# Kernel tuning notes

Hardware: AMD Instinct MI355X
Metric: run time of the kernel (lower is better)

The kernel has to match this reference:

```python
import jax, jax.numpy as jnp
import numpy as np
from jax import lax

# hyperparameters (match init_kwargs)
N_INP, N_HID, N_OUT = 3, 64, 10
SEQ_LEN, N_ROLL, K = 8, 16, 3
DT, GAMMA, EPS = 0.042, 2.7, 4.7
H, W = 12, 10            # hard-coded in coRNNCell2's PixelwiseConv2d
PAD = (K - 1) // 2
BATCH = 16


def setup_inputs() -> dict:
    key = jax.random.key(0)
    ks = jax.random.split(key, 7)
    x = jax.random.normal(ks[0], (SEQ_LEN, BATCH, N_INP, H, W), dtype=jnp.float32)
    # readin: Conv2d(seq_len*n_inp -> 2*n_hid, k, padding=1, replicate)
    readin_w = jax.random.normal(ks[1], (2 * N_HID, SEQ_LEN * N_INP, K, K), dtype=jnp.float32) * 0.05
    readin_b = jax.random.normal(ks[2], (2 * N_HID,), dtype=jnp.float32) * 0.05
    # PixelwiseConv2d: per-output-pixel weights (out, in, k, k, H, W)
    pw_w = jax.random.normal(ks[3], (N_HID, 2 * N_HID, K, K, H, W), dtype=jnp.float32) * 0.05
    pw_b = jax.random.normal(ks[4], (N_HID, H, W), dtype=jnp.float32) * 0.05
    # readout: 1x1 conv (n_hid -> n_out)
    readout_w = jax.random.normal(ks[5], (N_OUT, N_HID), dtype=jnp.float32) * 0.05
    readout_b = jax.random.normal(ks[6], (N_OUT,), dtype=jnp.float32) * 0.05
    return {"x": x, "readin_w": readin_w, "readin_b": readin_b,
            "pw_w": pw_w, "pw_b": pw_b,
            "readout_w": readout_w, "readout_b": readout_b}


def _pixelwise_conv(x, pw_w, pw_b):
    # x: (B, 2*N_HID, H, W); zero padding like F.unfold(padding=PAD)
    B = x.shape[0]
    xp = jnp.pad(x, ((0, 0), (0, 0), (PAD, PAD), (PAD, PAD)))
    # patches ordered (c, i, j) to match unfold().view(B, C, k, k, H, W)
    patches = jnp.stack([xp[:, :, i:i + H, j:j + W]
                         for i in range(K) for j in range(K)], axis=2)
    patches = patches.reshape(B, 2 * N_HID, K, K, H, W)
    return jnp.einsum('bcijhw,ocijhw->bohw', patches, pw_w) + pw_b[None]


def reference(x, readin_w, readin_b, pw_w, pw_b, readout_w, readout_b):
    T, B = x.shape[0], x.shape[1]
    # 't b c h w -> b (t c) h w'
    xr = jnp.transpose(x, (1, 0, 2, 3, 4)).reshape(B, T * N_INP, H, W)
    # readin conv with replicate padding
    xr_p = jnp.pad(xr, ((0, 0), (0, 0), (PAD, PAD), (PAD, PAD)), mode='edge')
    h = lax.conv_general_dilated(xr_p, readin_w, (1, 1), 'VALID',
                                 dimension_numbers=('NCHW', 'OIHW', 'NCHW'))
    h = h + readin_b[None, :, None, None]
    hy, hz = h[:, :N_HID], h[:, N_HID:]

    def step(carry, _):
        hy, hz = carry
        pre = _pixelwise_conv(jnp.concatenate([hz, hy], axis=1), pw_w, pw_b)
        hz = hz + DT * (jnp.tanh(pre) - GAMMA * hy - EPS * hz)
        hy = hy + DT * hz
        return (hy, hz), None

    (hy, hz), _ = lax.scan(step, (hy, hz), None, length=N_ROLL)
    out = jnp.einsum('bchw,oc->bohw', hy, readout_w) + readout_b[None, :, None, None]
    return out
```

## Files before the change

### kernel.cpp

```cpp
#include <hip/hip_runtime.h>
#include <math.h>

#define N_INPC 3
#define N_HID 64
#define N_OUTC 10
#define SEQ_LEN 8
#define N_ROLL 16
#define DT 0.042f
#define GAMMA 2.7f
#define EPSC 4.7f
#define HH 12
#define WW 10
#define NPIX 120
#define BATCH 16
#define NC 128
#define NK 1152

typedef __attribute__((ext_vector_type(8))) short short8;
typedef __attribute__((ext_vector_type(4))) float f32x4;
typedef unsigned short ushort_t;
typedef unsigned long long u64;

__device__ __forceinline__ ushort_t f2bf(float v) {
  union { float f; unsigned u; } x; x.f = v;
  unsigned r = x.u + 0x7fff + ((x.u >> 16) & 1);
  return (ushort_t)(r >> 16);
}

__global__ __launch_bounds__(256) void transpose2_kernel(
    const float* __restrict__ pw_w, ushort_t* __restrict__ Wt) {
  const int t = blockIdx.x * 256 + threadIdx.x;
  if (t >= 120 * 9216) return;
  const int p = t % 120;
  const int rest = t / 120;
  const int o = rest & 15;
  const int kg = (rest >> 4) & 3;
  const int ks = (rest >> 6) % 36;
  const int T = (rest >> 6) / 36;
  const int o_g = T * 16 + o;
  const int k0 = ks * 32 + kg * 8;
  ushort_t out8[8];
#pragma unroll
  for (int j = 0; j < 8; ++j) {
    const int kp = k0 + j;
    const int ij = kp >> 7;
    const int c = kp & 127;
    out8[j] = f2bf(pw_w[((size_t)o_g * NK + c * 9 + ij) * NPIX + p]);
  }
  uint4 pack;
  pack.x = (unsigned)out8[0] | ((unsigned)out8[1] << 16);
  pack.y = (unsigned)out8[2] | ((unsigned)out8[3] << 16);
  pack.z = (unsigned)out8[4] | ((unsigned)out8[5] << 16);
  pack.w = (unsigned)out8[6] | ((unsigned)out8[7] << 16);
  *(uint4*)(Wt + ((size_t)p * 9216 + rest) * 8) = pack;
}

__global__ __launch_bounds__(512, 1) void persist6_kernel(
    const ushort_t* __restrict__ Wt, ushort_t* __restrict__ SgA,
    ushort_t* __restrict__ SgB, const float* __restrict__ x,
    const float* __restrict__ rw, const float* __restrict__ rb,
    const float* __restrict__ pwb, const float* __restrict__ row,
    const float* __restrict__ rob, float* __restrict__ out,
    int* __restrict__ flags) {
  __shared__ char shraw[36864] __attribute__((aligned(16)));
  short8* SA = (short8*)shraw;
  float (*Sf)[128] = (float(*)[128])shraw;
  float (*hyf)[64] = (float(*)[64])shraw;
  __shared__ f32x4 red[256];
  __shared__ ushort_t tmp[16][128];

  const int p = blockIdx.x;
  const int ph = p / WW, pw_ = p % WW;
  const int tid = threadIdx.x, wv = tid >> 6, l = tid & 63;
  const int ot = wv & 3, kq = wv >> 2;
  const int kg = l >> 4, c16 = l & 15;
  const int o_g = ot * 16 + c16;
  const int b0 = (l >> 4) * 4;

  bool relevant = false;
  int faddr = 0;
  if (wv == 0 && l < 8) {
    const int q = l + (l >= 4);
    const int nh = ph + q / 3 - 1, nw = pw_ + q % 3 - 1;
    if ((unsigned)nh < (unsigned)HH && (unsigned)nw < (unsigned)WW) {
      relevant = true;
      faddr = (nh * WW + nw) * 16;
    }
  }

  {
    const int c = tid & 127;
    const int bq = tid >> 7;
    const int oc = (c < 64) ? (64 + c) : (c - 64);
    int ihs[3], iws[3];
#pragma unroll
    for (int d = 0; d < 3; ++d) {
      int ih = ph + d - 1; ihs[d] = ih < 0 ? 0 : (ih > HH - 1 ? HH - 1 : ih);
      int iw = pw_ + d - 1; iws[d] = iw < 0 ? 0 : (iw > WW - 1 ? WW - 1 : iw);
    }
    float a[4];
#pragma unroll
    for (int j = 0; j < 4; ++j) a[j] = rb[oc];
    for (int ch = 0; ch < SEQ_LEN * N_INPC; ++ch) {
      const int tt = ch / N_INPC, ic = ch % N_INPC;
      const float* wb = rw + (oc * (SEQ_LEN * N_INPC) + ch) * 9;
      float w9[9];
#pragma unroll
      for (int t2 = 0; t2 < 9; ++t2) w9[t2] = wb[t2];
#pragma unroll
      for (int j = 0; j < 4; ++j) {
        const float* xb =
            x + (((size_t)(tt * BATCH + bq * 4 + j) * N_INPC + ic) * HH) * WW;
        float s = 0.f;
#pragma unroll
        for (int di = 0; di < 3; ++di)
#pragma unroll
          for (int dj = 0; dj < 3; ++dj)
            s += xb[ihs[di] * WW + iws[dj]] * w9[di * 3 + dj];
        a[j] += s;
      }
    }
#pragma unroll
    for (int j = 0; j < 4; ++j) Sf[bq * 4 + j][c] = a[j];
  }
  __syncthreads();

  float hzr[4], hyr[4];
  if (wv < 4) {
#pragma unroll
    for (int r = 0; r < 4; ++r) {
      hzr[r] = Sf[b0 + r][o_g];
      hyr[r] = Sf[b0 + r][64 + o_g];
      tmp[b0 + r][o_g] = f2bf(hzr[r]);
      tmp[b0 + r][64 + o_g] = f2bf(hyr[r]);
    }
  }
  __syncthreads();

  {
    const int b = tid >> 5, ci = tid & 31;
    union { ushort_t us[4]; u64 u; } pk;
#pragma unroll
    for (int j2 = 0; j2 < 4; ++j2) pk.us[j2] = tmp[b][ci * 4 + j2];
    u64* dst = (u64*)(SgA + ((size_t)(p * BATCH + b)) * NC + ci * 4);
    __hip_atomic_store(dst, pk.u, __ATOMIC_RELAXED, __HIP_MEMORY_SCOPE_AGENT);
  }
  __syncthreads();
  if (tid == 0)
    __hip_atomic_store(flags + p * 16, 0, __ATOMIC_RELAXED,
                       __HIP_MEMORY_SCOPE_AGENT);

  short8 breg[18];
  {
    const short8* __restrict__ WB =
        (const short8*)Wt + ((size_t)(p * 4 + ot)) * 2304 + kg * 16 + c16;
#pragma unroll
    for (int j = 0; j < 18; ++j) breg[j] = WB[(size_t)(kq * 18 + j) * 64];
  }
  const float pb = pwb[o_g * NPIX + p];

  const int half = tid >> 8;
  const int hb = (tid >> 4) & 15;
  const int m = tid & 15;
  const int bm = hb * NC + m * 8;

  for (int s = 0; s < N_ROLL; ++s) {
    const ushort_t* __restrict__ sgc = (s & 1) ? SgB : SgA;
    ushort_t* __restrict__ sgn = (s & 1) ? SgA : SgB;

    if (wv == 0) {
      while (true) {
        int f = 0x7fffffff;
        if (relevant)
          f = __hip_atomic_load(flags + faddr, __ATOMIC_RELAXED,
                                __HIP_MEMORY_SCOPE_AGENT);
        if (__all(!relevant || f >= s)) break;
        __builtin_amdgcn_s_sleep(1);
      }
    }
    __syncthreads();

#pragma unroll
    for (int i = 0; i < 5; ++i) {
      if (half == 0 || i < 4) {
        const int q = 2 * i + half;
        short8 v;
        if (half == 0 && i == 2) {
          v = *(const short8*)&tmp[hb][m * 8];
        } else {
          const int ih = ph + q / 3 - 1, iw = pw_ + q % 3 - 1;
          union { u64 u[2]; short8 s8; } cv;
          cv.u[0] = 0; cv.u[1] = 0;
          if ((unsigned)ih < (unsigned)HH && (unsigned)iw < (unsigned)WW) {
            const u64* src =
                (const u64*)(sgc + (size_t)(ih * WW + iw) * (BATCH * NC) + bm);
            cv.u[0] = __hip_atomic_load(src, __ATOMIC_RELAXED,
                                        __HIP_MEMORY_SCOPE_AGENT);
            cv.u[1] = __hip_atomic_load(src + 1, __ATOMIC_RELAXED,
                                        __HIP_MEMORY_SCOPE_AGENT);
          }
          v = cv.s8;
        }
        const int rw_ = q * 16 + m;
        SA[rw_ * 16 + (hb ^ m)] = v;
      }
    }
    __syncthreads();

    f32x4 acc0 = {0.f, 0.f, 0.f, 0.f}, acc1 = {0.f, 0.f, 0.f, 0.f};
#pragma unroll
    for (int ii = 0; ii < 9; ++ii) {
      const int ks0 = kq * 18 + ii * 2;
      {
        const int r_ = ks0 * 4 + kg;
        acc0 = __builtin_amdgcn_mfma_f32_16x16x32_bf16(
            SA[r_ * 16 + (c16 ^ (r_ & 15))], breg[ii * 2], acc0, 0, 0, 0);
      }
      {
        const int r_ = (ks0 + 1) * 4 + kg;
        acc1 = __builtin_amdgcn_mfma_f32_16x16x32_bf16(
            SA[r_ * 16 + (c16 ^ (r_ & 15))], breg[ii * 2 + 1], acc1, 0, 0, 0);
      }
    }
    f32x4 acc = acc0 + acc1;

    if (wv >= 4) red[(wv - 4) * 64 + l] = acc;
    __syncthreads();
    if (wv < 4) {
      acc += red[wv * 64 + l];
#pragma unroll
      for (int r = 0; r < 4; ++r) {
        const float pre = acc[r] + pb;
        const float hz = hzr[r], hy = hyr[r];
        const float hzn = hz + DT * (tanhf(pre) - GAMMA * hy - EPSC * hz);
        const float hyn = hy + DT * hzn;
        hzr[r] = hzn;
        hyr[r] = hyn;
        if (s < N_ROLL - 1) {
          tmp[b0 + r][o_g] = f2bf(hzn);
          tmp[b0 + r][64 + o_g] = f2bf(hyn);
        }
      }
    }

    if (s < N_ROLL - 1) {
      __syncthreads();
      {
        const int b = tid >> 5, ci = tid & 31;
        union { ushort_t us[4]; u64 u; } pk;
#pragma unroll
        for (int j2 = 0; j2 < 4; ++j2) pk.us[j2] = tmp[b][ci * 4 + j2];
        u64* dst = (u64*)(sgn + ((size_t)(p * BATCH + b)) * NC + ci * 4);
        __hip_atomic_store(dst, pk.u, __ATOMIC_RELAXED,
                           __HIP_MEMORY_SCOPE_AGENT);
      }
      __syncthreads();
      if (tid == 0)
        __hip_atomic_store(flags + p * 16, s + 1, __ATOMIC_RELAXED,
                           __HIP_MEMORY_SCOPE_AGENT);
    }
  }

  __syncthreads();
  if (wv < 4) {
#pragma unroll
    for (int r = 0; r < 4; ++r) hyf[b0 + r][o_g] = hyr[r];
  }
  __syncthreads();
  if (tid < BATCH * N_OUTC) {
    const int b = tid / N_OUTC, o = tid % N_OUTC;
    float acc2 = rob[o];
#pragma unroll 8
    for (int c2 = 0; c2 < 64; ++c2) acc2 += hyf[b][c2] * row[o * 64 + c2];
    out[((size_t)(b * N_OUTC + o)) * NPIX + p] = acc2;
  }
}

extern "C" void kernel_launch(void* const* d_in, const int* in_sizes, int n_in,
                              void* d_out, int out_size, void* d_ws, size_t ws_size,
                              hipStream_t stream) {
  const float* x         = (const float*)d_in[0];
  const float* readin_w  = (const float*)d_in[1];
  const float* readin_b  = (const float*)d_in[2];
  const float* pw_w      = (const float*)d_in[3];
  const float* pw_b      = (const float*)d_in[4];
  const float* readout_w = (const float*)d_in[5];
  const float* readout_b = (const float*)d_in[6];
  float* out = (float*)d_out;

  ushort_t* Wt  = (ushort_t*)d_ws;
  ushort_t* Sg0 = Wt + (size_t)120 * 9216 * 8;
  ushort_t* Sg1 = Sg0 + 245760;
  int*      flg = (int*)(Sg1 + 245760);

  transpose2_kernel<<<4320, 256, 0, stream>>>(pw_w, Wt);

  {
    const ushort_t* aWt = Wt;
    ushort_t* aSgA = Sg0;
    ushort_t* aSgB = Sg1;
    const float* aX = x;
    const float* aRw = readin_w;
    const float* aRb = readin_b;
    const float* aPwb = pw_b;
    const float* aRow = readout_w;
    const float* aRob = readout_b;
    float* aOut = out;
    int* aFlg = flg;
    void* args[] = {(void*)&aWt, (void*)&aSgA, (void*)&aSgB, (void*)&aX,
                    (void*)&aRw, (void*)&aRb,  (void*)&aPwb, (void*)&aRow,
                    (void*)&aRob, (void*)&aOut, (void*)&aFlg};
    hipLaunchCooperativeKernel((const void*)persist6_kernel, dim3(NPIX),
                               dim3(512), args, 0, stream);
  }
}
```

Baseline: 202.2 us.

## Fuse weight transpose into persistent kernel and stream neighbor state straight into MFMA

Drops the separate transpose kernel: each block now reads its own pixel's fp32 weights, converts them to bf16 and keeps all 36 K-slices in registers. The block shrinks from 512 to 256 threads, so each wave owns one 16-output tile over the full K range and the cross-wave reduction through shared memory goes away. Neighbor state is loaded from global memory directly into MFMA operands, replacing the shared-memory staging and two barriers per step. The costs are heavier register pressure (36 short8 of weights), strided uncoalesced fp32 weight reads inside the timed kernel, and global-load latency sitting directly in front of the MFMA chain.

```diff
diff --git a/kernel.cpp b/kernel.cpp
--- a/kernel.cpp
+++ b/kernel.cpp
@@ -27,70 +27,52 @@
   return (ushort_t)(r >> 16);
 }
 
-__global__ __launch_bounds__(256) void transpose2_kernel(
-    const float* __restrict__ pw_w, ushort_t* __restrict__ Wt) {
-  const int t = blockIdx.x * 256 + threadIdx.x;
-  if (t >= 120 * 9216) return;
-  const int p = t % 120;
-  const int rest = t / 120;
-  const int o = rest & 15;
-  const int kg = (rest >> 4) & 3;
-  const int ks = (rest >> 6) % 36;
-  const int T = (rest >> 6) / 36;
-  const int o_g = T * 16 + o;
-  const int k0 = ks * 32 + kg * 8;
-  ushort_t out8[8];
-#pragma unroll
-  for (int j = 0; j < 8; ++j) {
-    const int kp = k0 + j;
-    const int ij = kp >> 7;
-    const int c = kp & 127;
-    out8[j] = f2bf(pw_w[((size_t)o_g * NK + c * 9 + ij) * NPIX + p]);
-  }
-  uint4 pack;
-  pack.x = (unsigned)out8[0] | ((unsigned)out8[1] << 16);
-  pack.y = (unsigned)out8[2] | ((unsigned)out8[3] << 16);
-  pack.z = (unsigned)out8[4] | ((unsigned)out8[5] << 16);
-  pack.w = (unsigned)out8[6] | ((unsigned)out8[7] << 16);
-  *(uint4*)(Wt + ((size_t)p * 9216 + rest) * 8) = pack;
-}
-
-__global__ __launch_bounds__(512, 1) void persist6_kernel(
-    const ushort_t* __restrict__ Wt, ushort_t* __restrict__ SgA,
-    ushort_t* __restrict__ SgB, const float* __restrict__ x,
-    const float* __restrict__ rw, const float* __restrict__ rb,
+__global__ __launch_bounds__(256, 1) void persist7_kernel(
+    ushort_t* __restrict__ SgA, ushort_t* __restrict__ SgB,
+    const float* __restrict__ x, const float* __restrict__ rw,
+    const float* __restrict__ rb, const float* __restrict__ pw_w,
     const float* __restrict__ pwb, const float* __restrict__ row,
     const float* __restrict__ rob, float* __restrict__ out,
     int* __restrict__ flags) {
-  __shared__ char shraw[36864] __attribute__((aligned(16)));
-  short8* SA = (short8*)shraw;
-  float (*Sf)[128] = (float(*)[128])shraw;
-  float (*hyf)[64] = (float(*)[64])shraw;
-  __shared__ f32x4 red[256];
+  __shared__ float Sf[16][128];
   __shared__ ushort_t tmp[16][128];
+  __shared__ float hyf[16][64];
 
   const int p = blockIdx.x;
   const int ph = p / WW, pw_ = p % WW;
   const int tid = threadIdx.x, wv = tid >> 6, l = tid & 63;
-  const int ot = wv & 3, kq = wv >> 2;
   const int kg = l >> 4, c16 = l & 15;
-  const int o_g = ot * 16 + c16;
-  const int b0 = (l >> 4) * 4;
-
-  bool relevant = false;
-  int faddr = 0;
-  if (wv == 0 && l < 8) {
+  const int o_g = wv * 16 + c16;
+  const int b0 = kg * 4;
+
+  bool rel = false;
+  int fadd = 0;
+  if (l < 8) {
     const int q = l + (l >= 4);
     const int nh = ph + q / 3 - 1, nw = pw_ + q % 3 - 1;
     if ((unsigned)nh < (unsigned)HH && (unsigned)nw < (unsigned)WW) {
-      relevant = true;
-      faddr = (nh * WW + nw) * 16;
-    }
-  }
+      rel = true;
+      fadd = (nh * WW + nw) * 16;
+    }
+  }
+
+  short8 breg[36];
+#pragma unroll
+  for (int ks = 0; ks < 36; ++ks) {
+    union { ushort_t us[8]; short8 s8; } pk;
+#pragma unroll
+    for (int j = 0; j < 8; ++j) {
+      const int kp = ks * 32 + kg * 8 + j;
+      const int ij = kp >> 7, c = kp & 127;
+      pk.us[j] = f2bf(pw_w[((size_t)o_g * NK + c * 9 + ij) * NPIX + p]);
+    }
+    breg[ks] = pk.s8;
+  }
+  const float pb = pwb[o_g * NPIX + p];
 
   {
     const int c = tid & 127;
-    const int bq = tid >> 7;
+    const int bh = tid >> 7;
     const int oc = (c < 64) ? (64 + c) : (c - 64);
     int ihs[3], iws[3];
 #pragma unroll
@@ -98,9 +80,9 @@
       int ih = ph + d - 1; ihs[d] = ih < 0 ? 0 : (ih > HH - 1 ? HH - 1 : ih);
       int iw = pw_ + d - 1; iws[d] = iw < 0 ? 0 : (iw > WW - 1 ? WW - 1 : iw);
     }
-    float a[4];
-#pragma unroll
-    for (int j = 0; j < 4; ++j) a[j] = rb[oc];
+    float a8[8];
+#pragma unroll
+    for (int j = 0; j < 8; ++j) a8[j] = rb[oc];
     for (int ch = 0; ch < SEQ_LEN * N_INPC; ++ch) {
       const int tt = ch / N_INPC, ic = ch % N_INPC;
       const float* wb = rw + (oc * (SEQ_LEN * N_INPC) + ch) * 9;
@@ -108,150 +90,113 @@
 #pragma unroll
       for (int t2 = 0; t2 < 9; ++t2) w9[t2] = wb[t2];
 #pragma unroll
-      for (int j = 0; j < 4; ++j) {
+      for (int j = 0; j < 8; ++j) {
         const float* xb =
-            x + (((size_t)(tt * BATCH + bq * 4 + j) * N_INPC + ic) * HH) * WW;
+            x + (((size_t)(tt * BATCH + bh * 8 + j) * N_INPC + ic) * HH) * WW;
         float s = 0.f;
 #pragma unroll
         for (int di = 0; di < 3; ++di)
 #pragma unroll
           for (int dj = 0; dj < 3; ++dj)
             s += xb[ihs[di] * WW + iws[dj]] * w9[di * 3 + dj];
-        a[j] += s;
-      }
-    }
-#pragma unroll
-    for (int j = 0; j < 4; ++j) Sf[bq * 4 + j][c] = a[j];
+        a8[j] += s;
+      }
+    }
+#pragma unroll
+    for (int j = 0; j < 8; ++j) Sf[bh * 8 + j][c] = a8[j];
   }
   __syncthreads();
 
   float hzr[4], hyr[4];
-  if (wv < 4) {
-#pragma unroll
-    for (int r = 0; r < 4; ++r) {
-      hzr[r] = Sf[b0 + r][o_g];
-      hyr[r] = Sf[b0 + r][64 + o_g];
-      tmp[b0 + r][o_g] = f2bf(hzr[r]);
-      tmp[b0 + r][64 + o_g] = f2bf(hyr[r]);
-    }
+#pragma unroll
+  for (int r = 0; r < 4; ++r) {
+    hzr[r] = Sf[b0 + r][o_g];
+    hyr[r] = Sf[b0 + r][64 + o_g];
+    tmp[b0 + r][o_g] = f2bf(hzr[r]);
+    tmp[b0 + r][64 + o_g] = f2bf(hyr[r]);
   }
   __syncthreads();
 
   {
-    const int b = tid >> 5, ci = tid & 31;
-    union { ushort_t us[4]; u64 u; } pk;
-#pragma unroll
-    for (int j2 = 0; j2 < 4; ++j2) pk.us[j2] = tmp[b][ci * 4 + j2];
-    u64* dst = (u64*)(SgA + ((size_t)(p * BATCH + b)) * NC + ci * 4);
-    __hip_atomic_store(dst, pk.u, __ATOMIC_RELAXED, __HIP_MEMORY_SCOPE_AGENT);
+    const int b = tid >> 4, m = tid & 15;
+    union { ushort_t us[8]; u64 u2[2]; } pk;
+#pragma unroll
+    for (int j = 0; j < 8; ++j) pk.us[j] = tmp[b][m * 8 + j];
+    u64* dst = (u64*)(SgA + ((size_t)(p * BATCH + b)) * NC + m * 8);
+    __hip_atomic_store(dst, pk.u2[0], __ATOMIC_RELAXED, __HIP_MEMORY_SCOPE_AGENT);
+    __hip_atomic_store(dst + 1, pk.u2[1], __ATOMIC_RELAXED, __HIP_MEMORY_SCOPE_AGENT);
   }
   __syncthreads();
   if (tid == 0)
     __hip_atomic_store(flags + p * 16, 0, __ATOMIC_RELAXED,
                        __HIP_MEMORY_SCOPE_AGENT);
 
-  short8 breg[18];
-  {
-    const short8* __restrict__ WB =
-        (const short8*)Wt + ((size_t)(p * 4 + ot)) * 2304 + kg * 16 + c16;
-#pragma unroll
-    for (int j = 0; j < 18; ++j) breg[j] = WB[(size_t)(kq * 18 + j) * 64];
-  }
-  const float pb = pwb[o_g * NPIX + p];
-
-  const int half = tid >> 8;
-  const int hb = (tid >> 4) & 15;
-  const int m = tid & 15;
-  const int bm = hb * NC + m * 8;
-
   for (int s = 0; s < N_ROLL; ++s) {
     const ushort_t* __restrict__ sgc = (s & 1) ? SgB : SgA;
     ushort_t* __restrict__ sgn = (s & 1) ? SgA : SgB;
 
-    if (wv == 0) {
-      while (true) {
-        int f = 0x7fffffff;
-        if (relevant)
-          f = __hip_atomic_load(flags + faddr, __ATOMIC_RELAXED,
-                                __HIP_MEMORY_SCOPE_AGENT);
-        if (__all(!relevant || f >= s)) break;
-        __builtin_amdgcn_s_sleep(1);
-      }
-    }
-    __syncthreads();
-
-#pragma unroll
-    for (int i = 0; i < 5; ++i) {
-      if (half == 0 || i < 4) {
-        const int q = 2 * i + half;
-        short8 v;
-        if (half == 0 && i == 2) {
-          v = *(const short8*)&tmp[hb][m * 8];
-        } else {
-          const int ih = ph + q / 3 - 1, iw = pw_ + q % 3 - 1;
-          union { u64 u[2]; short8 s8; } cv;
-          cv.u[0] = 0; cv.u[1] = 0;
-          if ((unsigned)ih < (unsigned)HH && (unsigned)iw < (unsigned)WW) {
-            const u64* src =
-                (const u64*)(sgc + (size_t)(ih * WW + iw) * (BATCH * NC) + bm);
-            cv.u[0] = __hip_atomic_load(src, __ATOMIC_RELAXED,
-                                        __HIP_MEMORY_SCOPE_AGENT);
-            cv.u[1] = __hip_atomic_load(src + 1, __ATOMIC_RELAXED,
-                                        __HIP_MEMORY_SCOPE_AGENT);
-          }
-          v = cv.s8;
-        }
-        const int rw_ = q * 16 + m;
-        SA[rw_ * 16 + (hb ^ m)] = v;
-      }
-    }
-    __syncthreads();
-
-    f32x4 acc0 = {0.f, 0.f, 0.f, 0.f}, acc1 = {0.f, 0.f, 0.f, 0.f};
-#pragma unroll
-    for (int ii = 0; ii < 9; ++ii) {
-      const int ks0 = kq * 18 + ii * 2;
-      {
-        const int r_ = ks0 * 4 + kg;
-        acc0 = __builtin_amdgcn_mfma_f32_16x16x32_bf16(
-            SA[r_ * 16 + (c16 ^ (r_ & 15))], breg[ii * 2], acc0, 0, 0, 0);
-      }
-      {
-        const int r_ = (ks0 + 1) * 4 + kg;
-        acc1 = __builtin_amdgcn_mfma_f32_16x16x32_bf16(
-            SA[r_ * 16 + (c16 ^ (r_ & 15))], breg[ii * 2 + 1], acc1, 0, 0, 0);
-      }
-    }
-    f32x4 acc = acc0 + acc1;
-
-    if (wv >= 4) red[(wv - 4) * 64 + l] = acc;
-    __syncthreads();
-    if (wv < 4) {
-      acc += red[wv * 64 + l];
-#pragma unroll
-      for (int r = 0; r < 4; ++r) {
-        const float pre = acc[r] + pb;
-        const float hz = hzr[r], hy = hyr[r];
-        const float hzn = hz + DT * (tanhf(pre) - GAMMA * hy - EPSC * hz);
-        const float hyn = hy + DT * hzn;
-        hzr[r] = hzn;
-        hyr[r] = hyn;
-        if (s < N_ROLL - 1) {
-          tmp[b0 + r][o_g] = f2bf(hzn);
-          tmp[b0 + r][64 + o_g] = f2bf(hyn);
-        }
+    while (true) {
+      int f = 0x7fffffff;
+      if (rel)
+        f = __hip_atomic_load(flags + fadd, __ATOMIC_RELAXED,
+                              __HIP_MEMORY_SCOPE_AGENT);
+      if (__all(!rel || f >= s)) break;
+      __builtin_amdgcn_s_sleep(1);
+    }
+    asm volatile("" ::: "memory");
+
+    f32x4 ac0 = {0.f, 0.f, 0.f, 0.f}, ac1 = {0.f, 0.f, 0.f, 0.f};
+    f32x4 ac2 = {0.f, 0.f, 0.f, 0.f}, ac3 = {0.f, 0.f, 0.f, 0.f};
+#pragma unroll
+    for (int ks = 0; ks < 36; ++ks) {
+      const int q = ks >> 2;
+      const int nh = ph + q / 3 - 1, nw = pw_ + q % 3 - 1;
+      short8 av = {0, 0, 0, 0, 0, 0, 0, 0};
+      if ((unsigned)nh < (unsigned)HH && (unsigned)nw < (unsigned)WW) {
+        const u64* src = (const u64*)(sgc +
+            (size_t)(nh * WW + nw) * (BATCH * NC) + c16 * NC +
+            ((ks & 3) * 32 + kg * 8));
+        union { u64 u[2]; short8 s8; } cv;
+        cv.u[0] = __hip_atomic_load(src, __ATOMIC_RELAXED,
+                                    __HIP_MEMORY_SCOPE_AGENT);
+        cv.u[1] = __hip_atomic_load(src + 1, __ATOMIC_RELAXED,
+                                    __HIP_MEMORY_SCOPE_AGENT);
+        av = cv.s8;
+      }
+      switch (ks & 3) {
+        case 0: ac0 = __builtin_amdgcn_mfma_f32_16x16x32_bf16(av, breg[ks], ac0, 0, 0, 0); break;
+        case 1: ac1 = __builtin_amdgcn_mfma_f32_16x16x32_bf16(av, breg[ks], ac1, 0, 0, 0); break;
+        case 2: ac2 = __builtin_amdgcn_mfma_f32_16x16x32_bf16(av, breg[ks], ac2, 0, 0, 0); break;
+        default: ac3 = __builtin_amdgcn_mfma_f32_16x16x32_bf16(av, breg[ks], ac3, 0, 0, 0); break;
+      }
+    }
+    f32x4 acc = (ac0 + ac1) + (ac2 + ac3);
+
+#pragma unroll
+    for (int r = 0; r < 4; ++r) {
+      const float pre = acc[r] + pb;
+      const float hz = hzr[r], hy = hyr[r];
+      const float hzn = hz + DT * (tanhf(pre) - GAMMA * hy - EPSC * hz);
+      const float hyn = hy + DT * hzn;
+      hzr[r] = hzn;
+      hyr[r] = hyn;
+      if (s < N_ROLL - 1) {
+        tmp[b0 + r][o_g] = f2bf(hzn);
+        tmp[b0 + r][64 + o_g] = f2bf(hyn);
       }
     }
 
     if (s < N_ROLL - 1) {
       __syncthreads();
       {
-        const int b = tid >> 5, ci = tid & 31;
-        union { ushort_t us[4]; u64 u; } pk;
-#pragma unroll
-        for (int j2 = 0; j2 < 4; ++j2) pk.us[j2] = tmp[b][ci * 4 + j2];
-        u64* dst = (u64*)(sgn + ((size_t)(p * BATCH + b)) * NC + ci * 4);
-        __hip_atomic_store(dst, pk.u, __ATOMIC_RELAXED,
+        const int b = tid >> 4, m = tid & 15;
+        union { ushort_t us[8]; u64 u2[2]; } pk;
+#pragma unroll
+        for (int j = 0; j < 8; ++j) pk.us[j] = tmp[b][m * 8 + j];
+        u64* dst = (u64*)(sgn + ((size_t)(p * BATCH + b)) * NC + m * 8);
+        __hip_atomic_store(dst, pk.u2[0], __ATOMIC_RELAXED,
+                           __HIP_MEMORY_SCOPE_AGENT);
+        __hip_atomic_store(dst + 1, pk.u2[1], __ATOMIC_RELAXED,
                            __HIP_MEMORY_SCOPE_AGENT);
       }
       __syncthreads();
@@ -262,10 +207,8 @@
   }
 
   __syncthreads();
-  if (wv < 4) {
-#pragma unroll
-    for (int r = 0; r < 4; ++r) hyf[b0 + r][o_g] = hyr[r];
-  }
+#pragma unroll
+  for (int r = 0; r < 4; ++r) hyf[b0 + r][o_g] = hyr[r];
   __syncthreads();
   if (tid < BATCH * N_OUTC) {
     const int b = tid / N_OUTC, o = tid % N_OUTC;
@@ -288,29 +231,28 @@
   const float* readout_b = (const float*)d_in[6];
   float* out = (float*)d_out;
 
-  ushort_t* Wt  = (ushort_t*)d_ws;
-  ushort_t* Sg0 = Wt + (size_t)120 * 9216 * 8;
+  ushort_t* Sg0 = (ushort_t*)d_ws;
   ushort_t* Sg1 = Sg0 + 245760;
   int*      flg = (int*)(Sg1 + 245760);
 
-  transpose2_kernel<<<4320, 256, 0, stream>>>(pw_w, Wt);
-
-  {
-    const ushort_t* aWt = Wt;
-    ushort_t* aSgA = Sg0;
-    ushort_t* aSgB = Sg1;
-    const float* aX = x;
-    const float* aRw = readin_w;
-    const float* aRb = readin_b;
-    const float* aPwb = pw_b;
-    const float* aRow = readout_w;
-    const float* aRob = readout_b;
-    float* aOut = out;
-    int* aFlg = flg;
-    void* args[] = {(void*)&aWt, (void*)&aSgA, (void*)&aSgB, (void*)&aX,
-                    (void*)&aRw, (void*)&aRb,  (void*)&aPwb, (void*)&aRow,
-                    (void*)&aRob, (void*)&aOut, (void*)&aFlg};
-    hipLaunchCooperativeKernel((const void*)persist6_kernel, dim3(NPIX),
-                               dim3(512), args, 0, stream);
+  ushort_t* aSgA = Sg0;
+  ushort_t* aSgB = Sg1;
+  const float* aX = x;
+  const float* aRw = readin_w;
+  const float* aRb = readin_b;
+  const float* aPw = pw_w;
+  const float* aPwb = pw_b;
+  const float* aRow = readout_w;
+  const float* aRob = readout_b;
+  float* aOut = out;
+  int* aFlg = flg;
+  void* args[] = {(void*)&aSgA, (void*)&aSgB, (void*)&aX,  (void*)&aRw,
+                  (void*)&aRb,  (void*)&aPw,  (void*)&aPwb, (void*)&aRow,
+                  (void*)&aRob, (void*)&aOut, (void*)&aFlg};
+  hipError_t rc = hipLaunchCooperativeKernel(
+      (const void*)persist7_kernel, dim3(NPIX), dim3(256), args, 0, stream);
+  if (rc != hipSuccess) {
+    persist7_kernel<<<dim3(NPIX), dim3(256), 0, stream>>>(
+        aSgA, aSgB, aX, aRw, aRb, aPw, aPwb, aRow, aRob, aOut, aFlg);
   }
 }
```

Measured after the change: 417.3 us. 2.06x slower.
